# Kernel optimization log

Hardware: AMD Instinct MI355X
Metric: run time of the kernel (lower is better)

## Reference

```python
import jax, jax.numpy as jnp
import numpy as np

N_NODES = 50000
N_FEAT = 256
HIDDEN = 256
N_EDGES = 800000


def gcn_conv(x, edge_index, W, b):
    """PyG GCNConv: out = D^-1/2 (A+I) D^-1/2 (x @ W) + b."""
    n = x.shape[0]
    loop = jnp.arange(n, dtype=edge_index.dtype)
    src = jnp.concatenate([edge_index[0], loop])  # [E+N]
    dst = jnp.concatenate([edge_index[1], loop])  # [E+N]
    deg = jax.ops.segment_sum(jnp.ones_like(dst, dtype=x.dtype), dst, num_segments=n)
    dinv = jnp.where(deg > 0, jax.lax.rsqrt(deg), 0.0)
    norm = dinv[src] * dinv[dst]                  # [E+N]
    h = x @ W                                     # [N, out]
    msg = h[src] * norm[:, None]                  # gather + scale
    out = jax.ops.segment_sum(msg, dst, num_segments=n)  # scatter-add
    return out + b


def setup_inputs() -> dict:
    key = jax.random.key(0)
    ks = jax.random.split(key, 8)
    x = jax.random.normal(ks[0], (N_NODES, N_FEAT), dtype=jnp.float32)
    train_pos_edge_index = jax.random.randint(ks[1], (2, N_EDGES), 0, N_NODES, dtype=jnp.int64)
    pos_edge_index = jax.random.randint(ks[2], (2, N_EDGES), 0, N_NODES, dtype=jnp.int64)
    neg_edge_index = jax.random.randint(ks[3], (2, N_EDGES), 0, N_NODES, dtype=jnp.int64)
    # Glorot-style init for GCN weights
    W1 = jax.random.normal(ks[4], (N_FEAT, HIDDEN), dtype=jnp.float32) * (1.0 / np.sqrt(N_FEAT))
    b1 = jnp.zeros((HIDDEN,), dtype=jnp.float32)
    W2 = jax.random.normal(ks[5], (HIDDEN, HIDDEN // 2), dtype=jnp.float32) * (1.0 / np.sqrt(HIDDEN))
    b2 = jnp.zeros((HIDDEN // 2,), dtype=jnp.float32)
    return {"x": x, "train_pos_edge_index": train_pos_edge_index,
            "pos_edge_index": pos_edge_index, "neg_edge_index": neg_edge_index,
            "W1": W1, "b1": b1, "W2": W2, "b2": b2}


def reference(x, train_pos_edge_index, pos_edge_index, neg_edge_index, W1, b1, W2, b2):
    # encode
    h = jax.nn.relu(gcn_conv(x, train_pos_edge_index, W1, b1))
    z = gcn_conv(h, train_pos_edge_index, W2, b2)  # [N, HIDDEN//2]
    # decode: dot product over concatenated pos+neg edges
    edge_index = jnp.concatenate([pos_edge_index, neg_edge_index], axis=-1)  # [2, 2E]
    logits = jnp.sum(z[edge_index[0]] * z[edge_index[1]], axis=-1)           # [2E]
    return logits
```

## Files before the change

kernel.cpp:

```cpp
#include <hip/hip_runtime.h>
#include <hip/hip_fp16.h>


#define NFEAT 256
#define HID   256
#define OUTF  128
#define SCAN_T 1024

typedef _Float16 f16x8 __attribute__((ext_vector_type(8)));
typedef float    f32x4 __attribute__((ext_vector_type(4)));

__global__ void k_init_deg(float* __restrict__ deg, int n) {
    int i = blockIdx.x * blockDim.x + threadIdx.x;
    if (i < n) deg[i] = 1.0f;
}

__global__ void k_count_deg(const int* __restrict__ ei, float* __restrict__ deg, int E) {
    int e = blockIdx.x * blockDim.x + threadIdx.x;
    if (e < E) atomicAdd(&deg[ei[E + e]], 1.0f);
}

__global__ __launch_bounds__(SCAN_T) void k_scan(
        float* __restrict__ deg_dinv, int* __restrict__ rowptr,
        int* __restrict__ cursor, int n) {
    __shared__ int swsum[16];
    __shared__ int s_total;
    __shared__ int s_chunk;
    const int t    = threadIdx.x;
    const int wave = t >> 6;
    const int lane = t & 63;
    if (t == 0) s_total = 0;

    for (int base = 0; base < n; base += SCAN_T) {
        int i = base + t;
        float dg = 1.0f;
        int v = 0;
        if (i < n) { dg = deg_dinv[i]; v = (int)dg - 1; }
        int sc = v;
#pragma unroll
        for (int off = 1; off < 64; off <<= 1) {
            int y = __shfl_up(sc, off);
            if (lane >= off) sc += y;
        }
        if (lane == 63) swsum[wave] = sc;
        __syncthreads();
        if (t < 16) {
            int w = swsum[t];
            int scw = w;
#pragma unroll
            for (int off = 1; off < 16; off <<= 1) {
                int y = __shfl_up(scw, off);
                if (t >= off) scw += y;
            }
            swsum[t] = scw - w;
            if (t == 15) s_chunk = scw;
        }
        __syncthreads();
        int rp = s_total + swsum[wave] + (sc - v);
        if (i < n) {
            rowptr[i] = rp;
            cursor[i] = rp;
            deg_dinv[i] = rsqrtf(dg);
        }
        __syncthreads();
        if (t == 0) s_total += s_chunk;
        __syncthreads();
    }
    if (t == 0) rowptr[n] = s_total;
}

__global__ void k_fill(const int* __restrict__ ei, int* __restrict__ cursor,
                       int* __restrict__ eidx, int E) {
    int e = blockIdx.x * blockDim.x + threadIdx.x;
    if (e < E) {
        int s = ei[e];
        int d = ei[E + e];
        int p = atomicAdd(&cursor[d], 1);
        eidx[p] = s;
    }
}

__global__ __launch_bounds__(256) void k_wt(const float* __restrict__ W,
                                            __half* __restrict__ Wt, int K, int M) {
    __shared__ float tile[32][33];
    int k0 = blockIdx.x * 32, m0 = blockIdx.y * 32;
    int tx = threadIdx.x & 31, ty = threadIdx.x >> 5;
#pragma unroll
    for (int r = 0; r < 4; ++r)
        tile[ty + r * 8][tx] = W[(size_t)(k0 + ty + r * 8) * M + m0 + tx];
    __syncthreads();
#pragma unroll
    for (int r = 0; r < 4; ++r)
        Wt[(size_t)(m0 + ty + r * 8) * K + k0 + tx] = __float2half(tile[tx][ty + r * 8]);
}

template <int MT, bool AF32, int SWL>
__global__ __launch_bounds__(256) void k_gemm_mfma(
        const void* __restrict__ Aptr, const __half* __restrict__ Wt,
        const float* __restrict__ dinv, __half* __restrict__ outp,
        int n, int K, int M) {
    constexpr int BM = 2 * MT * 16;
    __shared__ __half As[BM][40];
    __shared__ __half Bs[128][40];
    __shared__ __half Cs[4][16][72];

    const int t    = threadIdx.x;
    const int wave = t >> 6;
    const int lane = t & 63;
    const int row0 = blockIdx.x * BM;
    const int col0 = blockIdx.y * 128;
    const int wm = wave >> 1, wn = wave & 1;
    const int lr = lane & 15;
    const int kq = lane >> 4;

    f32x4 acc[MT][4];
#pragma unroll
    for (int i = 0; i < MT; ++i)
#pragma unroll
        for (int j = 0; j < 4; ++j) acc[i][j] = (f32x4){0.f, 0.f, 0.f, 0.f};

    for (int k0 = 0; k0 < K; k0 += 32) {
        if (AF32) {
            const float* A = (const float*)Aptr;
#pragma unroll
            for (int it = 0; it < BM * 8 / 256; ++it) {
                int q = t + it * 256;
                int r = q >> 3, c4 = q & 7;
                int gr = min(row0 + r, n - 1);
                float4 v = *(const float4*)&A[(size_t)gr * K + k0 + c4 * 4];
                __half2* dst = (__half2*)&As[r][c4 * 4];
                dst[0] = __floats2half2_rn(v.x, v.y);
                dst[1] = __floats2half2_rn(v.z, v.w);
            }
        } else {
            const __half* A = (const __half*)Aptr;
#pragma unroll
            for (int it = 0; it < BM * 4 / 256; ++it) {
                int q = t + it * 256;
                int r = q >> 2, c8 = q & 3;
                int gr = min(row0 + r, n - 1);
                *(float4*)&As[r][c8 * 8] = *(const float4*)&A[(size_t)gr * K + k0 + c8 * 8];
            }
        }
#pragma unroll
        for (int it = 0; it < 2; ++it) {
            int q = t + it * 256;
            int r = q >> 2, c8 = q & 3;
            *(float4*)&Bs[r][c8 * 8] = *(const float4*)&Wt[(size_t)(col0 + r) * K + k0 + c8 * 8];
        }
        __syncthreads();

        f16x8 b[4];
#pragma unroll
        for (int j = 0; j < 4; ++j)
            b[j] = *(const f16x8*)&Bs[wn * 64 + j * 16 + lr][kq * 8];
#pragma unroll
        for (int i = 0; i < MT; ++i) {
            f16x8 a = *(const f16x8*)&As[wm * MT * 16 + i * 16 + lr][kq * 8];
#pragma unroll
            for (int j = 0; j < 4; ++j)
                acc[i][j] = __builtin_amdgcn_mfma_f32_16x16x32_f16(a, b[j], acc[i][j], 0, 0, 0);
        }
        __syncthreads();
    }

    constexpr int SW = 1 << SWL;
#pragma unroll
    for (int i = 0; i < MT; ++i) {
        int gr0 = row0 + wm * MT * 16 + i * 16;
        float dv[4];
#pragma unroll
        for (int r = 0; r < 4; ++r)
            dv[r] = dinv[min(gr0 + kq * 4 + r, n - 1)];
        __syncthreads();
#pragma unroll
        for (int j = 0; j < 4; ++j)
#pragma unroll
            for (int r = 0; r < 4; ++r)
                Cs[wave][kq * 4 + r][j * 16 + lr] = __float2half(acc[i][j][r] * dv[r]);
        __syncthreads();
        int r1 = lane >> 3, c1 = (lane & 7) * 8;
#pragma unroll
        for (int h = 0; h < 2; ++h) {
            int grow = gr0 + r1 + h * 8;
            if (grow < n) {
                int col = col0 + wn * 64 + c1;
                size_t oidx = ((size_t)(col >> SWL) * n + grow) * SW + (col & (SW - 1));
                *(float4*)&outp[oidx] = *(const float4*)&Cs[wave][r1 + h * 8][c1];
            }
        }
    }
}

__global__ __launch_bounds__(256) void k_agg1(
        const int* __restrict__ rowptr, const int* __restrict__ eidx,
        const __half* __restrict__ g, const float* __restrict__ dinv,
        const float* __restrict__ bias, __half* __restrict__ out, int n) {
    const int node = (int)(((size_t)blockIdx.x * blockDim.x + threadIdx.x) >> 6);
    const int lane = threadIdx.x & 63;
    const int half = lane >> 5;
    const int fl   = lane & 31;
    if (node >= n) return;
    const int j0  = rowptr[node];
    const int end = rowptr[node + 1];
    const int last = end - 1;

    union U { float4 f; __half2 h[4]; };
    float acc[8] = {0.f, 0.f, 0.f, 0.f, 0.f, 0.f, 0.f, 0.f};
    {
        if (half == 0) {
            U u; u.f = *(const float4*)&g[(size_t)node * HID + fl * 8];
#pragma unroll
            for (int k = 0; k < 4; ++k) {
                float2 v = __half22float2(u.h[k]);
                acc[k * 2] += v.x; acc[k * 2 + 1] += v.y;
            }
        }
    }
    if (j0 < end) {
        int s0 = eidx[min(j0 + half, last)];
        int s1 = eidx[min(j0 + 2 + half, last)];
        for (int j = j0; j < end; j += 4) {
            int p0 = eidx[min(j + 4 + half, last)];
            int p1 = eidx[min(j + 6 + half, last)];
            U u0, u1;
            u0.f = *(const float4*)&g[(size_t)s0 * HID + fl * 8];
            u1.f = *(const float4*)&g[(size_t)s1 * HID + fl * 8];
            if (j + half < end) {
#pragma unroll
                for (int k = 0; k < 4; ++k) {
                    float2 v = __half22float2(u0.h[k]);
                    acc[k * 2] += v.x; acc[k * 2 + 1] += v.y;
                }
            }
            if (j + 2 + half < end) {
#pragma unroll
                for (int k = 0; k < 4; ++k) {
                    float2 v = __half22float2(u1.h[k]);
                    acc[k * 2] += v.x; acc[k * 2 + 1] += v.y;
                }
            }
            s0 = p0; s1 = p1;
        }
    }
#pragma unroll
    for (int k = 0; k < 8; ++k) acc[k] += __shfl_xor(acc[k], 32);
    if (half == 0) {
        const float sc = dinv[node];
        const int f0 = fl * 8;
        U r;
#pragma unroll
        for (int k = 0; k < 4; ++k) {
            float2 bb = *(const float2*)&bias[f0 + k * 2];
            r.h[k] = __floats2half2_rn(fmaxf(sc * acc[k * 2]     + bb.x, 0.f),
                                       fmaxf(sc * acc[k * 2 + 1] + bb.y, 0.f));
        }
        *(float4*)&out[(size_t)node * HID + f0] = r.f;
    }
}

__global__ __launch_bounds__(256) void k_agg2(
        const int* __restrict__ rowptr, const int* __restrict__ eidx,
        const __half* __restrict__ g, const float* __restrict__ dinv,
        const float* __restrict__ bias, __half* __restrict__ out, int n) {
    const int node = (int)(((size_t)blockIdx.x * blockDim.x + threadIdx.x) >> 6);
    const int lane = threadIdx.x & 63;
    const int q    = lane >> 4;
    const int fl   = lane & 15;
    if (node >= n) return;
    const int j0  = rowptr[node];
    const int end = rowptr[node + 1];
    const int last = end - 1;

    union U { float4 f; __half2 h[4]; };
    float acc[8] = {0.f, 0.f, 0.f, 0.f, 0.f, 0.f, 0.f, 0.f};
    if (q == 0) {
        U u; u.f = *(const float4*)&g[(size_t)node * OUTF + fl * 8];
#pragma unroll
        for (int k = 0; k < 4; ++k) {
            float2 v = __half22float2(u.h[k]);
            acc[k * 2] += v.x; acc[k * 2 + 1] += v.y;
        }
    }
    if (j0 < end) {
        int s0 = eidx[min(j0 + q, last)];
        for (int j = j0; j < end; j += 4) {
            int p0 = eidx[min(j + 4 + q, last)];
            U u0; u0.f = *(const float4*)&g[(size_t)s0 * OUTF + fl * 8];
            if (j + q < end) {
#pragma unroll
                for (int k = 0; k < 4; ++k) {
                    float2 v = __half22float2(u0.h[k]);
                    acc[k * 2] += v.x; acc[k * 2 + 1] += v.y;
                }
            }
            s0 = p0;
        }
    }
#pragma unroll
    for (int k = 0; k < 8; ++k) {
        acc[k] += __shfl_xor(acc[k], 16);
        acc[k] += __shfl_xor(acc[k], 32);
    }
    if (q == 0) {
        const float sc = dinv[node];
        const int f0 = fl * 8;
        U r;
#pragma unroll
        for (int k = 0; k < 4; ++k) {
            float2 bb = *(const float2*)&bias[f0 + k * 2];
            r.h[k] = __floats2half2_rn(sc * acc[k * 2]     + bb.x,
                                       sc * acc[k * 2 + 1] + bb.y);
        }
        *(float4*)&out[(size_t)node * OUTF + f0] = r.f;
    }
}

__global__ void k_decode(const int* __restrict__ pos, const int* __restrict__ neg,
                         const __half* __restrict__ z, float* __restrict__ out, int E) {
    size_t gid = (size_t)blockIdx.x * blockDim.x + threadIdx.x;
    int e  = (int)(gid >> 4);
    int sl = (int)(threadIdx.x & 15);
    if (e >= 2 * E) return;
    int a, b;
    if (e < E) { a = pos[e];     b = pos[E + e]; }
    else       { a = neg[e - E]; b = neg[e];     }
    union HF4 { float4 f; __half2 h[4]; };
    HF4 ua, ub;
    ua.f = ((const float4*)(z + (size_t)a * OUTF))[sl];
    ub.f = ((const float4*)(z + (size_t)b * OUTF))[sl];
    float p = 0.f;
#pragma unroll
    for (int k = 0; k < 4; ++k) {
        float2 fa = __half22float2(ua.h[k]);
        float2 fb = __half22float2(ub.h[k]);
        p = fmaf(fa.x, fb.x, p);
        p = fmaf(fa.y, fb.y, p);
    }
    p += __shfl_xor(p, 1);
    p += __shfl_xor(p, 2);
    p += __shfl_xor(p, 4);
    p += __shfl_xor(p, 8);
    if (sl == 0) out[e] = p;
}

extern "C" void kernel_launch(void* const* d_in, const int* in_sizes, int n_in,
                              void* d_out, int out_size, void* d_ws, size_t ws_size,
                              hipStream_t stream) {
    const float* x   = (const float*)d_in[0];
    const int*   tei = (const int*)d_in[1];
    const int*   pos = (const int*)d_in[2];
    const int*   neg = (const int*)d_in[3];
    const float* W1  = (const float*)d_in[4];
    const float* b1  = (const float*)d_in[5];
    const float* W2  = (const float*)d_in[6];
    const float* b2  = (const float*)d_in[7];
    float* out = (float*)d_out;

    const int N = in_sizes[0] / NFEAT;
    const int E = in_sizes[1] / 2;

    char* ws = (char*)d_ws;
    size_t off = 0;
    __half* g1h = (__half*)(ws + off);
    __half* g2h = (__half*)(ws + off);
    __half* zh  = (__half*)(ws + off + (size_t)N * OUTF * 2);
    off += (size_t)N * HID * 2;
    __half* h1h = (__half*)(ws + off);  off += (size_t)N * HID * 2;
    float*  dinv = (float*)(ws + off);  off += (size_t)N * 4;
    int* rowptr = (int*)(ws + off);     off += (size_t)(N + 1) * 4;
    int* cursor = (int*)(ws + off);     off += (size_t)N * 4;
    int* eidx   = (int*)(ws + off);     off += (size_t)E * 4;
    __half* W1t = (__half*)(ws + off);  off += (size_t)NFEAT * HID * 2;
    __half* W2t = (__half*)(ws + off);  off += (size_t)HID * OUTF * 2;

    { dim3 g(NFEAT / 32, HID / 32);  k_wt<<<g, 256, 0, stream>>>(W1, W1t, NFEAT, HID); }
    { dim3 g(HID / 32, OUTF / 32);   k_wt<<<g, 256, 0, stream>>>(W2, W2t, HID, OUTF); }

    k_init_deg<<<(N + 255) / 256, 256, 0, stream>>>(dinv, N);
    k_count_deg<<<(E + 255) / 256, 256, 0, stream>>>(tei, dinv, E);
    k_scan<<<1, SCAN_T, 0, stream>>>(dinv, rowptr, cursor, N);
    k_fill<<<(E + 255) / 256, 256, 0, stream>>>(tei, cursor, eidx, E);

    {
        dim3 grid((N + 127) / 128, HID / 128);
        k_gemm_mfma<4, true, 8><<<grid, 256, 0, stream>>>(x, W1t, dinv, g1h, N, NFEAT, HID);
        int nblk = (int)(((size_t)N * 64 + 255) / 256);
        k_agg1<<<nblk, 256, 0, stream>>>(rowptr, eidx, g1h, dinv, b1, h1h, N);
    }

    {
        dim3 grid((N + 63) / 64, OUTF / 128);
        k_gemm_mfma<2, false, 7><<<grid, 256, 0, stream>>>(h1h, W2t, dinv, g2h, N, HID, OUTF);
        int nblk = (int)(((size_t)N * 64 + 255) / 256);
        k_agg2<<<nblk, 256, 0, stream>>>(rowptr, eidx, g2h, dinv, b2, zh, N);
    }

    {
        size_t nth = (size_t)2 * E * 16;
        k_decode<<<(int)((nth + 255) / 256), 256, 0, stream>>>(pos, neg, zh, out, E);
    }
}
```

Measured before the change: 474.6 us.

## Replace single-block degree scan with three-pass multi-block scan

New measurement: 429.4 us. 9.5% less time.

```diff
diff --git a/kernel.cpp b/kernel.cpp
--- a/kernel.cpp
+++ b/kernel.cpp
@@ -5,7 +5,6 @@
 #define NFEAT 256
 #define HID   256
 #define OUTF  128
-#define SCAN_T 1024
 
 typedef _Float16 f16x8 __attribute__((ext_vector_type(8)));
 typedef float    f32x4 __attribute__((ext_vector_type(4)));
@@ -20,53 +19,61 @@
     if (e < E) atomicAdd(&deg[ei[E + e]], 1.0f);
 }
 
-__global__ __launch_bounds__(SCAN_T) void k_scan(
-        float* __restrict__ deg_dinv, int* __restrict__ rowptr,
-        int* __restrict__ cursor, int n) {
+__global__ __launch_bounds__(1024) void k_scan1(
+        const float* __restrict__ deg, int* __restrict__ excl,
+        int* __restrict__ bsum, int n) {
     __shared__ int swsum[16];
-    __shared__ int s_total;
-    __shared__ int s_chunk;
-    const int t    = threadIdx.x;
-    const int wave = t >> 6;
-    const int lane = t & 63;
-    if (t == 0) s_total = 0;
-
-    for (int base = 0; base < n; base += SCAN_T) {
-        int i = base + t;
-        float dg = 1.0f;
-        int v = 0;
-        if (i < n) { dg = deg_dinv[i]; v = (int)dg - 1; }
-        int sc = v;
-#pragma unroll
-        for (int off = 1; off < 64; off <<= 1) {
-            int y = __shfl_up(sc, off);
-            if (lane >= off) sc += y;
-        }
-        if (lane == 63) swsum[wave] = sc;
-        __syncthreads();
-        if (t < 16) {
-            int w = swsum[t];
-            int scw = w;
-#pragma unroll
-            for (int off = 1; off < 16; off <<= 1) {
-                int y = __shfl_up(scw, off);
-                if (t >= off) scw += y;
-            }
-            swsum[t] = scw - w;
-            if (t == 15) s_chunk = scw;
-        }
-        __syncthreads();
-        int rp = s_total + swsum[wave] + (sc - v);
-        if (i < n) {
-            rowptr[i] = rp;
-            cursor[i] = rp;
-            deg_dinv[i] = rsqrtf(dg);
-        }
-        __syncthreads();
-        if (t == 0) s_total += s_chunk;
-        __syncthreads();
-    }
-    if (t == 0) rowptr[n] = s_total;
+    const int t = threadIdx.x, wave = t >> 6, lane = t & 63;
+    const int i = blockIdx.x * 1024 + t;
+    int v = (i < n) ? (int)deg[i] - 1 : 0;
+    int sc = v;
+#pragma unroll
+    for (int off = 1; off < 64; off <<= 1) {
+        int y = __shfl_up(sc, off);
+        if (lane >= off) sc += y;
+    }
+    if (lane == 63) swsum[wave] = sc;
+    __syncthreads();
+    if (t < 16) {
+        int w = swsum[t];
+        int scw = w;
+#pragma unroll
+        for (int off = 1; off < 16; off <<= 1) {
+            int y = __shfl_up(scw, off);
+            if (t >= off) scw += y;
+        }
+        swsum[t] = scw - w;
+        if (t == 15) bsum[blockIdx.x] = scw;
+    }
+    __syncthreads();
+    if (i < n) excl[i] = swsum[wave] + (sc - v);
+}
+
+__global__ void k_scan2(int* __restrict__ bsum, int nb) {
+    int t = threadIdx.x;
+    int v = (t < nb) ? bsum[t] : 0;
+    int sc = v;
+#pragma unroll
+    for (int off = 1; off < 64; off <<= 1) {
+        int y = __shfl_up(sc, off);
+        if (t >= off) sc += y;
+    }
+    if (t < nb) bsum[t] = sc - v;
+    if (t == 63) bsum[nb] = sc;
+}
+
+__global__ void k_scan3(float* __restrict__ deg_dinv, const int* __restrict__ excl,
+                        const int* __restrict__ bsum, int* __restrict__ rowptr,
+                        int* __restrict__ cursor, int n, int nb) {
+    int i = blockIdx.x * blockDim.x + threadIdx.x;
+    if (i < n) {
+        int rp = excl[i] + bsum[i >> 10];
+        rowptr[i] = rp;
+        cursor[i] = rp;
+        deg_dinv[i] = rsqrtf(deg_dinv[i]);
+    } else if (i == n) {
+        rowptr[n] = bsum[nb];
+    }
 }
 
 __global__ void k_fill(const int* __restrict__ ei, int* __restrict__ cursor,
@@ -359,6 +366,7 @@
 
     const int N = in_sizes[0] / NFEAT;
     const int E = in_sizes[1] / 2;
+    const int NB = (N + 1023) / 1024;
 
     char* ws = (char*)d_ws;
     size_t off = 0;
@@ -373,13 +381,17 @@
     int* eidx   = (int*)(ws + off);     off += (size_t)E * 4;
     __half* W1t = (__half*)(ws + off);  off += (size_t)NFEAT * HID * 2;
     __half* W2t = (__half*)(ws + off);  off += (size_t)HID * OUTF * 2;
+    int* excl   = (int*)(ws + off);     off += (size_t)N * 4;
+    int* bsum   = (int*)(ws + off);     off += (size_t)(NB + 1) * 4;
 
     { dim3 g(NFEAT / 32, HID / 32);  k_wt<<<g, 256, 0, stream>>>(W1, W1t, NFEAT, HID); }
     { dim3 g(HID / 32, OUTF / 32);   k_wt<<<g, 256, 0, stream>>>(W2, W2t, HID, OUTF); }
 
     k_init_deg<<<(N + 255) / 256, 256, 0, stream>>>(dinv, N);
     k_count_deg<<<(E + 255) / 256, 256, 0, stream>>>(tei, dinv, E);
-    k_scan<<<1, SCAN_T, 0, stream>>>(dinv, rowptr, cursor, N);
+    k_scan1<<<NB, 1024, 0, stream>>>(dinv, excl, bsum, N);
+    k_scan2<<<1, 64, 0, stream>>>(bsum, NB);
+    k_scan3<<<(N + 256) / 256, 256, 0, stream>>>(dinv, excl, bsum, rowptr, cursor, N, NB);
     k_fill<<<(E + 255) / 256, 256, 0, stream>>>(tei, cursor, eidx, E);
 
     {
```
